# Performance work log

Hardware: AMD Instinct MI355X
Metric: run time of the kernel (lower is better)

## Reference

```python
import jax, jax.numpy as jnp
import numpy as np

HIDDEN = 1024
FFN = 2048
N_EXPERTS = 8
TOP_K = 2


def setup_inputs() -> dict:
    key = jax.random.key(0)
    k_x, k_g, k1, k2, k3 = jax.random.split(key, 5)
    hidden_states = jax.random.normal(k_x, (4, 4096, HIDDEN), dtype=jnp.float32)
    gate_w = jax.random.normal(k_g, (N_EXPERTS, HIDDEN), dtype=jnp.float32) * 0.02
    # nn.Linear convention: weight is [out_features, in_features]
    w1 = jax.random.normal(k1, (N_EXPERTS, FFN, HIDDEN), dtype=jnp.float32) * 0.02
    w2 = jax.random.normal(k2, (N_EXPERTS, HIDDEN, FFN), dtype=jnp.float32) * 0.02
    w3 = jax.random.normal(k3, (N_EXPERTS, FFN, HIDDEN), dtype=jnp.float32) * 0.02
    return {"hidden_states": hidden_states, "gate_w": gate_w, "w1": w1, "w2": w2, "w3": w3}


def reference(hidden_states, gate_w, w1, w2, w3):
    B, S, H = hidden_states.shape
    E = gate_w.shape[0]
    x = hidden_states.reshape(-1, H)  # [T, H]
    T = x.shape[0]

    # Router: softmax in fp32, top-2, renormalize (matches torch reference)
    router_logits = jnp.einsum("th,eh->te", x, gate_w)
    probs = jax.nn.softmax(router_logits.astype(jnp.float32), axis=-1)
    top_w, top_i = jax.lax.top_k(probs, TOP_K)  # [T, 2]
    top_w = top_w / jnp.sum(top_w, axis=-1, keepdims=True)
    top_w = top_w.astype(x.dtype)

    # Dense combine weights [T, E]: zero for unselected experts.
    combine = jnp.zeros((T, E), dtype=x.dtype)
    combine = combine.at[jnp.arange(T)[:, None], top_i].set(top_w)

    # Per-expert SwiGLU; loop over small fixed expert count, accumulate.
    out = jnp.zeros_like(x)
    for e in range(E):
        h = jax.nn.silu(x @ w1[e].T) * (x @ w3[e].T)  # [T, FFN]
        out = out + combine[:, e:e + 1] * (h @ w2[e].T)
    return out.reshape(B, S, H)
```

## Files before the change

kernel.cpp:

```cpp
#include <hip/hip_runtime.h>
#include <cstdint>

#define H 1024
#define F 2048
#define E_N 8
#define BM 256
#define BK 64
#define NW (E_N * F * H)

typedef __attribute__((ext_vector_type(8))) short short8v;
typedef __attribute__((ext_vector_type(4))) float float4v;
typedef unsigned short u16;

__device__ __forceinline__ u16 f2bf(float f) {
    uint32_t u = __float_as_uint(f);
    u += 0x7FFFu + ((u >> 16) & 1u);
    return (u16)(u >> 16);
}
__device__ __forceinline__ float bf2f(u16 b) {
    return __uint_as_float(((uint32_t)b) << 16);
}

__device__ __forceinline__ void gload16(const void* g, void* l) {
    __builtin_amdgcn_global_load_lds((const __attribute__((address_space(1))) uint32_t*)g,
                                     (__attribute__((address_space(3))) uint32_t*)l, 16, 0, 0);
}

__device__ __forceinline__ void barx() {
    asm volatile("" ::: "memory");
    __builtin_amdgcn_s_barrier();
    asm volatile("" ::: "memory");
}

__device__ __forceinline__ void decode_swz(int bid, int nTiles, int ngy, int gyc,
                                           int& tile, int& gy) {
    int nblk = nTiles * ngy;
    int q = nblk >> 3, r = nblk & 7;
    int xcd = bid & 7, pos = bid >> 3;
    int cid = (xcd < r ? xcd * (q + 1) : r * (q + 1) + (xcd - r) * q) + pos;
    int per = nTiles * gyc;
    int chunk = cid / per, rem = cid - chunk * per;
    tile = rem / gyc;
    gy = chunk * gyc + (rem - (rem / gyc) * gyc);
}

__global__ __launch_bounds__(256) void cvt3_kernel(const float* __restrict__ s0,
                                                   const float* __restrict__ s1,
                                                   const float* __restrict__ s2,
                                                   u16* __restrict__ dst) {
    int i = (blockIdx.x * 256 + threadIdx.x) * 4;
    int stride = gridDim.x * 256 * 4;
    for (; i < 3 * NW; i += stride) {
        int seg = i / NW;
        int off = i - seg * NW;
        const float* s = (seg == 0) ? s0 : ((seg == 1) ? s1 : s2);
        float4 v = *(const float4*)(s + off);
        ushort4 o;
        o.x = f2bf(v.x); o.y = f2bf(v.y); o.z = f2bf(v.z); o.w = f2bf(v.w);
        *(ushort4*)(dst + i) = o;
    }
}

__global__ __launch_bounds__(256) void router_kernel(const float* __restrict__ x,
                                                     const float* __restrict__ gw,
                                                     int* __restrict__ topi,
                                                     float* __restrict__ topw,
                                                     u16* __restrict__ xg, int T) {
    int wave = threadIdx.x >> 6, lane = threadIdx.x & 63;
    int t = blockIdx.x * 4 + wave;
    if (t >= T) return;
    const float4* xr = (const float4*)(x + (size_t)t * H);
    float4 xv[4];
#pragma unroll
    for (int i = 0; i < 4; i++) xv[i] = xr[i * 64 + lane];
#pragma unroll
    for (int i = 0; i < 4; i++) {
        ushort4 o;
        o.x = f2bf(xv[i].x); o.y = f2bf(xv[i].y);
        o.z = f2bf(xv[i].z); o.w = f2bf(xv[i].w);
        *(ushort4*)(xg + (size_t)t * H + (i * 64 + lane) * 4) = o;
    }
    float acc[E_N];
#pragma unroll
    for (int e = 0; e < E_N; e++) {
        const float4* gr = (const float4*)(gw + e * H);
        float s = 0.f;
#pragma unroll
        for (int i = 0; i < 4; i++) {
            float4 g = gr[i * 64 + lane];
            s += xv[i].x * g.x + xv[i].y * g.y + xv[i].z * g.z + xv[i].w * g.w;
        }
        acc[e] = s;
    }
#pragma unroll
    for (int e = 0; e < E_N; e++) {
#pragma unroll
        for (int off = 32; off; off >>= 1) acc[e] += __shfl_xor(acc[e], off, 64);
    }
    if (lane == 0) {
        int i0 = 0;
#pragma unroll
        for (int e = 1; e < E_N; e++) if (acc[e] > acc[i0]) i0 = e;
        int i1 = -1;
#pragma unroll
        for (int e = 0; e < E_N; e++) {
            if (e == i0) continue;
            if (i1 < 0 || acc[e] > acc[i1]) i1 = e;
        }
        float e1 = __expf(acc[i1] - acc[i0]);
        float w0 = 1.f / (1.f + e1);
        float w1v = e1 / (1.f + e1);
        topi[t * 2] = i0; topi[t * 2 + 1] = i1;
        topw[t * 2] = w0; topw[t * 2 + 1] = w1v;
    }
}

__global__ __launch_bounds__(256) void hist_kernel(const int* __restrict__ topi,
                                                   int* __restrict__ counts, int n) {
    __shared__ int hc[E_N];
    if (threadIdx.x < E_N) hc[threadIdx.x] = 0;
    __syncthreads();
    for (int i = blockIdx.x * 256 + threadIdx.x; i < n; i += gridDim.x * 256)
        atomicAdd(&hc[topi[i]], 1);
    __syncthreads();
    if (threadIdx.x < E_N) atomicAdd(&counts[threadIdx.x], hc[threadIdx.x]);
}

__global__ void scan_kernel(const int* __restrict__ counts, int* __restrict__ offsets,
                            int* __restrict__ cursors, int* __restrict__ tileOff) {
    if (threadIdx.x == 0 && blockIdx.x == 0) {
        int o = 0, to = 0;
        for (int e = 0; e < E_N; e++) {
            offsets[e] = o; cursors[e] = o; tileOff[e] = to;
            o += counts[e];
            to += (counts[e] + BM - 1) / BM;
        }
        offsets[E_N] = o; tileOff[E_N] = to;
    }
}

__global__ __launch_bounds__(1024) void scatter_kernel(const int* __restrict__ topi,
                                                       const float* __restrict__ topw,
                                                       int* __restrict__ cursors,
                                                       int* __restrict__ perm_tok,
                                                       float* __restrict__ perm_gate,
                                                       int* __restrict__ inv, int n) {
    __shared__ int hc[E_N];
    __shared__ int base[E_N];
    int tid = threadIdx.x;
    if (tid < E_N) hc[tid] = 0;
    __syncthreads();
    int i = blockIdx.x * 1024 + tid;
    int e = 0, lrank = 0;
    bool ok = (i < n);
    if (ok) {
        e = topi[i];
        lrank = atomicAdd(&hc[e], 1);
    }
    __syncthreads();
    if (tid < E_N) base[tid] = atomicAdd(&cursors[tid], hc[tid]);
    __syncthreads();
    if (ok) {
        int pos = base[e] + lrank;
        perm_tok[pos] = i >> 1;
        perm_gate[pos] = topw[i];
        inv[i] = pos;
    }
}

__global__ __launch_bounds__(512) void stage1_kernel(
    const u16* __restrict__ xg, const u16* __restrict__ w1b, const u16* __restrict__ w3b,
    const int* __restrict__ perm_tok, const float* __restrict__ perm_gate,
    const int* __restrict__ offsets, const int* __restrict__ tileOff,
    u16* __restrict__ h, int cstart, int tpcThis) {
    __shared__ u16 lA[2 * BM * BK];
    __shared__ u16 lB1[2 * 128 * BK];
    __shared__ u16 lB3[2 * 128 * BK];
    __shared__ int ptokS[BM];
    __shared__ float pgateS[BM];

    int tileL, nbIdx;
    decode_swz(blockIdx.x, tpcThis, F / 128, 4, tileL, nbIdx);
    int tile = cstart + tileL;
    if (tile >= tileOff[E_N]) return;
    int e = 0;
    while (e < E_N - 1 && tile >= tileOff[e + 1]) e++;
    int rbase = offsets[e] + (tile - tileOff[e]) * BM;
    int segEnd = offsets[e + 1];
    int e0 = 0;
    while (e0 < E_N - 1 && cstart >= tileOff[e0 + 1]) e0++;
    int chunkBase = offsets[e0] + (cstart - tileOff[e0]) * BM;

    int tid = threadIdx.x;
    if (tid < BM) {
        int p = rbase + tid; if (p > segEnd - 1) p = segEnd - 1;
        ptokS[tid] = perm_tok[p];
        pgateS[tid] = perm_gate[p];
    }
    __syncthreads();

    int lane = tid & 63, wid = tid >> 6;
    int wr = wid >> 2, wc = wid & 3;
    int lrow = lane & 15, kgrp = lane >> 4;
    int lr = lane >> 3, csw = ((lane & 7) ^ lr) << 3;
    int nb = nbIdx * 128;
    const u16* w1p = w1b + (size_t)e * F * H + (size_t)nb * H;
    const u16* w3p = w3b + (size_t)e * F * H + (size_t)nb * H;

    const u16* pA[4];
#pragma unroll
    for (int j = 0; j < 4; j++) pA[j] = xg + (size_t)ptokS[(j * 8 + wid) * 8 + lr] * H + csw;
    const u16 *pB1[2], *pB3[2];
#pragma unroll
    for (int j = 0; j < 2; j++) {
        int rr = (j * 8 + wid) * 8 + lr;
        pB1[j] = w1p + (size_t)rr * H + csw;
        pB3[j] = w3p + (size_t)rr * H + csw;
    }

    int swe0 = (kgrp ^ (lrow & 7)) << 3;
    int swe1 = ((4 + kgrp) ^ (lrow & 7)) << 3;
    int eA0 = (wr * 128 + lrow) * BK + swe0;
    int eA1 = (wr * 128 + lrow) * BK + swe1;
    int eB0 = (wc * 32 + lrow) * BK + swe0;
    int eB1 = (wc * 32 + lrow) * BK + swe1;

#define STA(CC, j)  gload16(pA[j],  &lA[(CC) * 16384 + ((j) * 8 + wid) * 8 * BK])
#define STB1(CC, j) gload16(pB1[j], &lB1[(CC) * 8192 + ((j) * 8 + wid) * 8 * BK])
#define STB3(CC, j) gload16(pB3[j], &lB3[(CC) * 8192 + ((j) * 8 + wid) * 8 * BK])

    float4v acc1[8][2], acc3[8][2];
#pragma unroll
    for (int a = 0; a < 8; a++)
#pragma unroll
        for (int b = 0; b < 2; b++) { acc1[a][b] = (float4v)(0.f); acc3[a][b] = (float4v)(0.f); }

    STB1(0, 0); STB1(0, 1);
    STB3(0, 0); STB3(0, 1);
    STA(0, 0); STA(0, 2); STA(0, 1); STA(0, 3);
#pragma unroll
    for (int j = 0; j < 4; j++) pA[j] += BK;
    pB1[0] += BK; pB1[1] += BK; pB3[0] += BK; pB3[1] += BK;
    asm volatile("s_waitcnt vmcnt(2)" ::: "memory");
    barx();

#define S1_DSA(CC, p) \
    short8v aF[2][2]; \
    _Pragma("unroll") \
    for (int pm = 0; pm < 2; pm++) { \
        aF[pm][0] = *(const short8v*)&lA[eA0 + (CC) * 16384 + (2 * (p) + pm) * 1024]; \
        aF[pm][1] = *(const short8v*)&lA[eA1 + (CC) * 16384 + (2 * (p) + pm) * 1024]; \
    }
#define S1_MM(p) \
    __builtin_amdgcn_s_setprio(1); \
    _Pragma("unroll") \
    for (int pm = 0; pm < 2; pm++) \
    _Pragma("unroll") \
    for (int n = 0; n < 2; n++) \
    _Pragma("unroll") \
    for (int kk = 0; kk < 2; kk++) { \
        acc1[2 * (p) + pm][n] = __builtin_amdgcn_mfma_f32_16x16x32_bf16(aF[pm][kk], b1F[n][kk], acc1[2 * (p) + pm][n], 0, 0, 0); \
        acc3[2 * (p) + pm][n] = __builtin_amdgcn_mfma_f32_16x16x32_bf16(aF[pm][kk], b3F[n][kk], acc3[2 * (p) + pm][n], 0, 0, 0); \
    } \
    __builtin_amdgcn_s_setprio(0);

#define S1_KT(CC, LAST) { \
    short8v b1F[2][2], b3F[2][2]; \
    _Pragma("unroll") \
    for (int n = 0; n < 2; n++) { \
        b1F[n][0] = *(const short8v*)&lB1[eB0 + (CC) * 8192 + n * 1024]; \
        b1F[n][1] = *(const short8v*)&lB1[eB1 + (CC) * 8192 + n * 1024]; \
        b3F[n][0] = *(const short8v*)&lB3[eB0 + (CC) * 8192 + n * 1024]; \
        b3F[n][1] = *(const short8v*)&lB3[eB1 + (CC) * 8192 + n * 1024]; \
    } \
    { S1_DSA(CC, 0) \
      if (!(LAST)) { STB1((CC) ^ 1, 0); STB1((CC) ^ 1, 1); STA((CC) ^ 1, 0); } \
      barx(); S1_MM(0) barx(); } \
    { S1_DSA(CC, 1) \
      if (!(LAST)) { STB3((CC) ^ 1, 0); STB3((CC) ^ 1, 1); STA((CC) ^ 1, 2); } \
      barx(); S1_MM(1) \
      if (!(LAST)) { asm volatile("s_waitcnt vmcnt(6)" ::: "memory"); } \
      else         { asm volatile("s_waitcnt vmcnt(0)" ::: "memory"); } \
      barx(); } \
    { S1_DSA(CC, 2) \
      if (!(LAST)) { STA((CC) ^ 1, 1); } \
      barx(); S1_MM(2) barx(); } \
    { S1_DSA(CC, 3) \
      if (!(LAST)) { STA((CC) ^ 1, 3); } \
      barx(); S1_MM(3) \
      asm volatile("s_waitcnt vmcnt(2)" ::: "memory"); \
      barx(); } \
    _Pragma("unroll") \
    for (int j = 0; j < 4; j++) pA[j] += BK; \
    pB1[0] += BK; pB1[1] += BK; pB3[0] += BK; pB3[1] += BK; \
}

    for (int tt = 0; tt < (H / BK) - 2; tt += 2) {
        S1_KT(0, false)
        S1_KT(1, false)
    }
    S1_KT(0, false)
    S1_KT(1, true)
#undef S1_DSA
#undef S1_MM
#undef S1_KT
#undef STA
#undef STB1
#undef STB3

    int rif = (lane >> 4) * 4;
#pragma unroll
    for (int m = 0; m < 8; m++) {
#pragma unroll
        for (int reg = 0; reg < 4; reg++) {
            int rowIdx = wr * 128 + m * 16 + rif + reg;
            int p = rbase + rowIdx;
            if (p < segEnd) {
                float g = pgateS[rowIdx];
#pragma unroll
                for (int n = 0; n < 2; n++) {
                    float a1 = acc1[m][n][reg], a3 = acc3[m][n][reg];
                    float sv = a1 / (1.f + __expf(-a1));
                    float hv = sv * a3 * g;
                    int ncol = nb + wc * 32 + n * 16 + (lane & 15);
                    h[(size_t)(p - chunkBase) * F + ncol] = f2bf(hv);
                }
            }
        }
    }
}

template<int NREP>
__global__ __launch_bounds__(512) void stage2_kernel(
    const u16* __restrict__ h, const u16* __restrict__ w2b,
    const int* __restrict__ offsets, const int* __restrict__ tileOff,
    u16* __restrict__ y, int cstart, int tpcThis) {
    constexpr int BN = NREP * 64;
    constexpr int BSTRIDE = BN * BK;
    __shared__ u16 lA[2 * BM * BK];
    __shared__ u16 lB[2 * BSTRIDE];

    int tileL, nbIdx;
    decode_swz(blockIdx.x, tpcThis, H / BN, 4, tileL, nbIdx);
    int tile = cstart + tileL;
    if (tile >= tileOff[E_N]) return;
    int e = 0;
    while (e < E_N - 1 && tile >= tileOff[e + 1]) e++;
    int rbase = offsets[e] + (tile - tileOff[e]) * BM;
    int segEnd = offsets[e + 1];
    int e0 = 0;
    while (e0 < E_N - 1 && cstart >= tileOff[e0 + 1]) e0++;
    int chunkBase = offsets[e0] + (cstart - tileOff[e0]) * BM;

    int tid = threadIdx.x;
    int lane = tid & 63, wid = tid >> 6;
    int wr = wid >> 2, wc = wid & 3;
    int lrow = lane & 15, kgrp = lane >> 4;
    int lr = lane >> 3, csw = ((lane & 7) ^ lr) << 3;
    int nb = nbIdx * BN;
    const u16* w2p = w2b + (size_t)e * H * F + (size_t)nb * F;

    const u16* pA[4];
#pragma unroll
    for (int j = 0; j < 4; j++) {
        int rb = (j * 8 + wid) * 8;
        int p = rbase + rb + lr; if (p > segEnd - 1) p = segEnd - 1;
        pA[j] = h + (size_t)(p - chunkBase) * F + csw;
    }
    const u16* pB[NREP];
#pragma unroll
    for (int j = 0; j < NREP; j++) pB[j] = w2p + (size_t)((j * 8 + wid) * 8 + lr) * F + csw;

    int swe0 = (kgrp ^ (lrow & 7)) << 3;
    int swe1 = ((4 + kgrp) ^ (lrow & 7)) << 3;
    int eA0 = (wr * 128 + lrow) * BK + swe0;
    int eA1 = (wr * 128 + lrow) * BK + swe1;
    int eB0 = (wc * (NREP * 16) + lrow) * BK + swe0;
    int eB1 = (wc * (NREP * 16) + lrow) * BK + swe1;

#define STA2(CC, j) gload16(pA[j], &lA[(CC) * 16384 + ((j) * 8 + wid) * 8 * BK])
#define STB2(CC, j) gload16(pB[j], &lB[(CC) * BSTRIDE + ((j) * 8 + wid) * 8 * BK])

    float4v acc[8][NREP];
#pragma unroll
    for (int a = 0; a < 8; a++)
#pragma unroll
        for (int b = 0; b < NREP; b++) acc[a][b] = (float4v)(0.f);

#pragma unroll
    for (int j = 0; j < NREP; j++) STB2(0, j);
    STA2(0, 0); STA2(0, 2); STA2(0, 1); STA2(0, 3);
#pragma unroll
    for (int j = 0; j < 4; j++) pA[j] += BK;
#pragma unroll
    for (int j = 0; j < NREP; j++) pB[j] += BK;
    asm volatile("s_waitcnt vmcnt(2)" ::: "memory");
    barx();

#define S2_DSA(CC, p) \
    short8v aF[2][2]; \
    _Pragma("unroll") \
    for (int pm = 0; pm < 2; pm++) { \
        aF[pm][0] = *(const short8v*)&lA[eA0 + (CC) * 16384 + (2 * (p) + pm) * 1024]; \
        aF[pm][1] = *(const short8v*)&lA[eA1 + (CC) * 16384 + (2 * (p) + pm) * 1024]; \
    }
#define S2_MM(p) \
    __builtin_amdgcn_s_setprio(1); \
    _Pragma("unroll") \
    for (int pm = 0; pm < 2; pm++) \
    _Pragma("unroll") \
    for (int n = 0; n < NREP; n++) \
    _Pragma("unroll") \
    for (int kk = 0; kk < 2; kk++) \
        acc[2 * (p) + pm][n] = __builtin_amdgcn_mfma_f32_16x16x32_bf16(aF[pm][kk], bF[n][kk], acc[2 * (p) + pm][n], 0, 0, 0); \
    __builtin_amdgcn_s_setprio(0);

#define S2_KT(CC, LAST) { \
    short8v bF[NREP][2]; \
    _Pragma("unroll") \
    for (int n = 0; n < NREP; n++) { \
        bF[n][0] = *(const short8v*)&lB[eB0 + (CC) * BSTRIDE + n * 1024]; \
        bF[n][1] = *(const short8v*)&lB[eB1 + (CC) * BSTRIDE + n * 1024]; \
    } \
    { S2_DSA(CC, 0) \
      if (!(LAST)) { STB2((CC) ^ 1, 0); if (NREP == 4) STB2((CC) ^ 1, 1); STA2((CC) ^ 1, 0); } \
      barx(); S2_MM(0) barx(); } \
    { S2_DSA(CC, 1) \
      if (!(LAST)) { if (NREP == 4) { STB2((CC) ^ 1, 2); STB2((CC) ^ 1, 3); } else STB2((CC) ^ 1, 1); \
                     STA2((CC) ^ 1, 2); } \
      barx(); S2_MM(1) \
      if (!(LAST)) { \
          if (NREP == 4) { asm volatile("s_waitcnt vmcnt(6)" ::: "memory"); } \
          else           { asm volatile("s_waitcnt vmcnt(4)" ::: "memory"); } \
      } else { asm volatile("s_waitcnt vmcnt(0)" ::: "memory"); } \
      barx(); } \
    { S2_DSA(CC, 2) \
      if (!(LAST)) { STA2((CC) ^ 1, 1); } \
      barx(); S2_MM(2) barx(); } \
    { S2_DSA(CC, 3) \
      if (!(LAST)) { STA2((CC) ^ 1, 3); } \
      barx(); S2_MM(3) \
      asm volatile("s_waitcnt vmcnt(2)" ::: "memory"); \
      barx(); } \
    _Pragma("unroll") \
    for (int j = 0; j < 4; j++) pA[j] += BK; \
    _Pragma("unroll") \
    for (int j = 0; j < NREP; j++) pB[j] += BK; \
}

    for (int tt = 0; tt < (F / BK) - 2; tt += 2) {
        S2_KT(0, false)
        S2_KT(1, false)
    }
    S2_KT(0, false)
    S2_KT(1, true)
#undef S2_DSA
#undef S2_MM
#undef S2_KT
#undef STA2
#undef STB2

    int rif = (lane >> 4) * 4;
#pragma unroll
    for (int m = 0; m < 8; m++) {
#pragma unroll
        for (int reg = 0; reg < 4; reg++) {
            int rowIdx = wr * 128 + m * 16 + rif + reg;
            int p = rbase + rowIdx;
            if (p < segEnd) {
#pragma unroll
                for (int n = 0; n < NREP; n++) {
                    int col = nb + wc * (BN / 4) + n * 16 + (lane & 15);
                    y[(size_t)p * H + col] = f2bf(acc[m][n][reg]);
                }
            }
        }
    }
}

__global__ __launch_bounds__(256) void combine_kernel(const u16* __restrict__ y,
                                                      const int* __restrict__ inv,
                                                      float* __restrict__ out) {
    int t = blockIdx.x, c = threadIdx.x;
    int s0 = inv[t * 2], s1 = inv[t * 2 + 1];
    ushort4 a = *(const ushort4*)(y + (size_t)s0 * H + c * 4);
    ushort4 b = *(const ushort4*)(y + (size_t)s1 * H + c * 4);
    float4 o;
    o.x = bf2f(a.x) + bf2f(b.x);
    o.y = bf2f(a.y) + bf2f(b.y);
    o.z = bf2f(a.z) + bf2f(b.z);
    o.w = bf2f(a.w) + bf2f(b.w);
    *(float4*)(out + (size_t)t * H + c * 4) = o;
}

extern "C" void kernel_launch(void* const* d_in, const int* in_sizes, int n_in,
                              void* d_out, int out_size, void* d_ws, size_t ws_size,
                              hipStream_t stream) {
    (void)n_in; (void)out_size;
    const float* x  = (const float*)d_in[0];
    const float* gw = (const float*)d_in[1];
    const float* w1 = (const float*)d_in[2];
    const float* w2 = (const float*)d_in[3];
    const float* w3 = (const float*)d_in[4];
    float* out = (float*)d_out;
    int T = in_sizes[0] / H;
    int P = T * 2;

    char* ws = (char*)d_ws;
    size_t off = 0;
    auto alloc = [&](size_t b) { size_t c = off; off = (off + b + 255) & ~(size_t)255; return c; };
    size_t misc_o  = alloc(256);
    int* counts  = (int*)(ws + misc_o);
    int* offsets = (int*)(ws + misc_o + 64);
    int* cursors = (int*)(ws + misc_o + 128);
    int* tileOff = (int*)(ws + misc_o + 192);
    size_t topi_o  = alloc((size_t)T * 2 * 4);
    size_t topw_o  = alloc((size_t)T * 2 * 4);
    size_t ptok_o  = alloc((size_t)P * 4);
    size_t pgate_o = alloc((size_t)P * 4);
    size_t inv_o   = alloc((size_t)T * 2 * 4);
    size_t wb_o  = alloc((size_t)3 * NW * 2);
    size_t xg_o  = alloc((size_t)T * H * 2);
    size_t y_o   = alloc((size_t)P * H * 2);
    u16* w1b = (u16*)(ws + wb_o);
    u16* w3b = w1b + NW;
    u16* w2b = w1b + 2 * (size_t)NW;

    int maxTiles = P / BM + E_N;
    size_t perTile = (size_t)BM * F * 2;
    size_t avail = (ws_size > off + 256) ? (ws_size - off - 256) : 0;
    int tpc = (int)(avail / perTile);
    if (tpc > maxTiles) tpc = maxTiles;
    if (tpc < 4) tpc = 4;
    size_t h_o = alloc((size_t)tpc * perTile);

    hipMemsetAsync(ws + misc_o, 0, 256, stream);

    cvt3_kernel<<<8192, 256, 0, stream>>>(w1, w3, w2, w1b);
    router_kernel<<<T / 4, 256, 0, stream>>>(x, gw, (int*)(ws + topi_o), (float*)(ws + topw_o),
                                             (u16*)(ws + xg_o), T);
    hist_kernel<<<32, 256, 0, stream>>>((int*)(ws + topi_o), counts, P);
    scan_kernel<<<1, 64, 0, stream>>>(counts, offsets, cursors, tileOff);
    scatter_kernel<<<(P + 1023) / 1024, 1024, 0, stream>>>(
        (int*)(ws + topi_o), (float*)(ws + topw_o), cursors,
        (int*)(ws + ptok_o), (float*)(ws + pgate_o), (int*)(ws + inv_o), P);

    for (int cstart = 0; cstart < maxTiles; cstart += tpc) {
        int tpcThis = maxTiles - cstart; if (tpcThis > tpc) tpcThis = tpc;
        stage1_kernel<<<tpcThis * (F / 128), 512, 0, stream>>>(
            (u16*)(ws + xg_o), w1b, w3b,
            (int*)(ws + ptok_o), (float*)(ws + pgate_o), offsets, tileOff,
            (u16*)(ws + h_o), cstart, tpcThis);
        if (tpcThis >= 54)
            stage2_kernel<4><<<tpcThis * (H / 256), 512, 0, stream>>>(
                (u16*)(ws + h_o), w2b, offsets, tileOff,
                (u16*)(ws + y_o), cstart, tpcThis);
        else
            stage2_kernel<2><<<tpcThis * (H / 128), 512, 0, stream>>>(
                (u16*)(ws + h_o), w2b, offsets, tileOff,
                (u16*)(ws + y_o), cstart, tpcThis);
    }
    combine_kernel<<<T, 256, 0, stream>>>((u16*)(ws + y_o), (int*)(ws + inv_o), out);
}
```

Measured before the change: 640.3 us.

## Switch stage1/stage2 GEMMs to 32x32x16 MFMA and balance chunk sizes

Replaces the 16x16x32 bf16 MFMA tiling in both expert GEMM kernels with 32x32x16 MFMA, restructuring LDS fragment loads, swizzle offsets, the K-loop into two half-phases with fewer barriers, and the epilogue row mapping. The larger MFMA needs fewer LDS fragment reads per FLOP and fewer instructions. The host also splits tiles evenly across chunks and changes the threshold for picking the wider stage2 variant. This risks higher register pressure from the 16-wide accumulators, and the epilogue writes are less coalesced.

After: 751.5 us. +17.4%, slower.

```diff
diff --git a/kernel.cpp b/kernel.cpp
--- a/kernel.cpp
+++ b/kernel.cpp
@@ -9,7 +9,7 @@
 #define NW (E_N * F * H)
 
 typedef __attribute__((ext_vector_type(8))) short short8v;
-typedef __attribute__((ext_vector_type(4))) float float4v;
+typedef __attribute__((ext_vector_type(16))) float float16v;
 typedef unsigned short u16;
 
 __device__ __forceinline__ u16 f2bf(float f) {
@@ -201,7 +201,7 @@
 
     int lane = tid & 63, wid = tid >> 6;
     int wr = wid >> 2, wc = wid & 3;
-    int lrow = lane & 15, kgrp = lane >> 4;
+    int l32 = lane & 31, hi = lane >> 5;
     int lr = lane >> 3, csw = ((lane & 7) ^ lr) << 3;
     int nb = nbIdx * 128;
     const u16* w1p = w1b + (size_t)e * F * H + (size_t)nb * H;
@@ -218,22 +218,19 @@
         pB3[j] = w3p + (size_t)rr * H + csw;
     }
 
-    int swe0 = (kgrp ^ (lrow & 7)) << 3;
-    int swe1 = ((4 + kgrp) ^ (lrow & 7)) << 3;
-    int eA0 = (wr * 128 + lrow) * BK + swe0;
-    int eA1 = (wr * 128 + lrow) * BK + swe1;
-    int eB0 = (wc * 32 + lrow) * BK + swe0;
-    int eB1 = (wc * 32 + lrow) * BK + swe1;
+    int uk[4];
+#pragma unroll
+    for (int k = 0; k < 4; k++) uk[k] = ((2 * k + hi) ^ (lane & 7)) << 3;
+    int aBase = (wr * 128 + l32) * BK;
+    int bBase = (wc * 32 + l32) * BK;
 
 #define STA(CC, j)  gload16(pA[j],  &lA[(CC) * 16384 + ((j) * 8 + wid) * 8 * BK])
 #define STB1(CC, j) gload16(pB1[j], &lB1[(CC) * 8192 + ((j) * 8 + wid) * 8 * BK])
 #define STB3(CC, j) gload16(pB3[j], &lB3[(CC) * 8192 + ((j) * 8 + wid) * 8 * BK])
 
-    float4v acc1[8][2], acc3[8][2];
-#pragma unroll
-    for (int a = 0; a < 8; a++)
-#pragma unroll
-        for (int b = 0; b < 2; b++) { acc1[a][b] = (float4v)(0.f); acc3[a][b] = (float4v)(0.f); }
+    float16v acc1[4], acc3[4];
+#pragma unroll
+    for (int a = 0; a < 4; a++) { acc1[a] = (float16v)(0.f); acc3[a] = (float16v)(0.f); }
 
     STB1(0, 0); STB1(0, 1);
     STB3(0, 0); STB3(0, 1);
@@ -244,52 +241,48 @@
     asm volatile("s_waitcnt vmcnt(2)" ::: "memory");
     barx();
 
-#define S1_DSA(CC, p) \
-    short8v aF[2][2]; \
-    _Pragma("unroll") \
-    for (int pm = 0; pm < 2; pm++) { \
-        aF[pm][0] = *(const short8v*)&lA[eA0 + (CC) * 16384 + (2 * (p) + pm) * 1024]; \
-        aF[pm][1] = *(const short8v*)&lA[eA1 + (CC) * 16384 + (2 * (p) + pm) * 1024]; \
-    }
-#define S1_MM(p) \
+#define S1_KT(CC, LAST) { \
+    short8v b1F[4], b3F[4], aF[2][4]; \
+    _Pragma("unroll") \
+    for (int k = 0; k < 4; k++) { \
+        b1F[k] = *(const short8v*)&lB1[(CC) * 8192 + bBase + uk[k]]; \
+        b3F[k] = *(const short8v*)&lB3[(CC) * 8192 + bBase + uk[k]]; \
+        aF[0][k] = *(const short8v*)&lA[(CC) * 16384 + aBase + uk[k]]; \
+        aF[1][k] = *(const short8v*)&lA[(CC) * 16384 + aBase + 2048 + uk[k]]; \
+    } \
+    if (!(LAST)) { STB1((CC) ^ 1, 0); STB1((CC) ^ 1, 1); STB3((CC) ^ 1, 0); STB3((CC) ^ 1, 1); \
+                   STA((CC) ^ 1, 0); STA((CC) ^ 1, 2); } \
+    barx(); \
     __builtin_amdgcn_s_setprio(1); \
     _Pragma("unroll") \
-    for (int pm = 0; pm < 2; pm++) \
-    _Pragma("unroll") \
-    for (int n = 0; n < 2; n++) \
-    _Pragma("unroll") \
-    for (int kk = 0; kk < 2; kk++) { \
-        acc1[2 * (p) + pm][n] = __builtin_amdgcn_mfma_f32_16x16x32_bf16(aF[pm][kk], b1F[n][kk], acc1[2 * (p) + pm][n], 0, 0, 0); \
-        acc3[2 * (p) + pm][n] = __builtin_amdgcn_mfma_f32_16x16x32_bf16(aF[pm][kk], b3F[n][kk], acc3[2 * (p) + pm][n], 0, 0, 0); \
-    } \
-    __builtin_amdgcn_s_setprio(0);
-
-#define S1_KT(CC, LAST) { \
-    short8v b1F[2][2], b3F[2][2]; \
-    _Pragma("unroll") \
-    for (int n = 0; n < 2; n++) { \
-        b1F[n][0] = *(const short8v*)&lB1[eB0 + (CC) * 8192 + n * 1024]; \
-        b1F[n][1] = *(const short8v*)&lB1[eB1 + (CC) * 8192 + n * 1024]; \
-        b3F[n][0] = *(const short8v*)&lB3[eB0 + (CC) * 8192 + n * 1024]; \
-        b3F[n][1] = *(const short8v*)&lB3[eB1 + (CC) * 8192 + n * 1024]; \
-    } \
-    { S1_DSA(CC, 0) \
-      if (!(LAST)) { STB1((CC) ^ 1, 0); STB1((CC) ^ 1, 1); STA((CC) ^ 1, 0); } \
-      barx(); S1_MM(0) barx(); } \
-    { S1_DSA(CC, 1) \
-      if (!(LAST)) { STB3((CC) ^ 1, 0); STB3((CC) ^ 1, 1); STA((CC) ^ 1, 2); } \
-      barx(); S1_MM(1) \
-      if (!(LAST)) { asm volatile("s_waitcnt vmcnt(6)" ::: "memory"); } \
-      else         { asm volatile("s_waitcnt vmcnt(0)" ::: "memory"); } \
-      barx(); } \
-    { S1_DSA(CC, 2) \
-      if (!(LAST)) { STA((CC) ^ 1, 1); } \
-      barx(); S1_MM(2) barx(); } \
-    { S1_DSA(CC, 3) \
-      if (!(LAST)) { STA((CC) ^ 1, 3); } \
-      barx(); S1_MM(3) \
-      asm volatile("s_waitcnt vmcnt(2)" ::: "memory"); \
-      barx(); } \
+    for (int k = 0; k < 4; k++) \
+    _Pragma("unroll") \
+    for (int mt = 0; mt < 2; mt++) { \
+        acc1[mt] = __builtin_amdgcn_mfma_f32_32x32x16_bf16(aF[mt][k], b1F[k], acc1[mt], 0, 0, 0); \
+        acc3[mt] = __builtin_amdgcn_mfma_f32_32x32x16_bf16(aF[mt][k], b3F[k], acc3[mt], 0, 0, 0); \
+    } \
+    __builtin_amdgcn_s_setprio(0); \
+    if (!(LAST)) { asm volatile("s_waitcnt vmcnt(6)" ::: "memory"); } \
+    else         { asm volatile("s_waitcnt vmcnt(0)" ::: "memory"); } \
+    barx(); \
+    _Pragma("unroll") \
+    for (int k = 0; k < 4; k++) { \
+        aF[0][k] = *(const short8v*)&lA[(CC) * 16384 + aBase + 2 * 2048 + uk[k]]; \
+        aF[1][k] = *(const short8v*)&lA[(CC) * 16384 + aBase + 3 * 2048 + uk[k]]; \
+    } \
+    if (!(LAST)) { STA((CC) ^ 1, 1); STA((CC) ^ 1, 3); } \
+    barx(); \
+    __builtin_amdgcn_s_setprio(1); \
+    _Pragma("unroll") \
+    for (int k = 0; k < 4; k++) \
+    _Pragma("unroll") \
+    for (int mt = 0; mt < 2; mt++) { \
+        acc1[2 + mt] = __builtin_amdgcn_mfma_f32_32x32x16_bf16(aF[mt][k], b1F[k], acc1[2 + mt], 0, 0, 0); \
+        acc3[2 + mt] = __builtin_amdgcn_mfma_f32_32x32x16_bf16(aF[mt][k], b3F[k], acc3[2 + mt], 0, 0, 0); \
+    } \
+    __builtin_amdgcn_s_setprio(0); \
+    asm volatile("s_waitcnt vmcnt(2)" ::: "memory"); \
+    barx(); \
     _Pragma("unroll") \
     for (int j = 0; j < 4; j++) pA[j] += BK; \
     pB1[0] += BK; pB1[1] += BK; pB3[0] += BK; pB3[1] += BK; \
@@ -301,30 +294,24 @@
     }
     S1_KT(0, false)
     S1_KT(1, true)
-#undef S1_DSA
-#undef S1_MM
 #undef S1_KT
 #undef STA
 #undef STB1
 #undef STB3
 
-    int rif = (lane >> 4) * 4;
-#pragma unroll
-    for (int m = 0; m < 8; m++) {
-#pragma unroll
-        for (int reg = 0; reg < 4; reg++) {
-            int rowIdx = wr * 128 + m * 16 + rif + reg;
+#pragma unroll
+    for (int mt = 0; mt < 4; mt++) {
+#pragma unroll
+        for (int r = 0; r < 16; r++) {
+            int rowIdx = wr * 128 + mt * 32 + (r & 3) + 8 * (r >> 2) + 4 * hi;
             int p = rbase + rowIdx;
             if (p < segEnd) {
                 float g = pgateS[rowIdx];
-#pragma unroll
-                for (int n = 0; n < 2; n++) {
-                    float a1 = acc1[m][n][reg], a3 = acc3[m][n][reg];
-                    float sv = a1 / (1.f + __expf(-a1));
-                    float hv = sv * a3 * g;
-                    int ncol = nb + wc * 32 + n * 16 + (lane & 15);
-                    h[(size_t)(p - chunkBase) * F + ncol] = f2bf(hv);
-                }
+                float a1 = acc1[mt][r], a3v = acc3[mt][r];
+                float sv = a1 / (1.f + __expf(-a1));
+                float hv = sv * a3v * g;
+                int ncol = nb + wc * 32 + l32;
+                h[(size_t)(p - chunkBase) * F + ncol] = f2bf(hv);
             }
         }
     }
@@ -337,6 +324,7 @@
     u16* __restrict__ y, int cstart, int tpcThis) {
     constexpr int BN = NREP * 64;
     constexpr int BSTRIDE = BN * BK;
+    constexpr int NT32 = NREP / 2;
     __shared__ u16 lA[2 * BM * BK];
     __shared__ u16 lB[2 * BSTRIDE];
 
@@ -355,7 +343,7 @@
     int tid = threadIdx.x;
     int lane = tid & 63, wid = tid >> 6;
     int wr = wid >> 2, wc = wid & 3;
-    int lrow = lane & 15, kgrp = lane >> 4;
+    int l32 = lane & 31, hi = lane >> 5;
     int lr = lane >> 3, csw = ((lane & 7) ^ lr) << 3;
     int nb = nbIdx * BN;
     const u16* w2p = w2b + (size_t)e * H * F + (size_t)nb * F;
@@ -371,21 +359,20 @@
 #pragma unroll
     for (int j = 0; j < NREP; j++) pB[j] = w2p + (size_t)((j * 8 + wid) * 8 + lr) * F + csw;
 
-    int swe0 = (kgrp ^ (lrow & 7)) << 3;
-    int swe1 = ((4 + kgrp) ^ (lrow & 7)) << 3;
-    int eA0 = (wr * 128 + lrow) * BK + swe0;
-    int eA1 = (wr * 128 + lrow) * BK + swe1;
-    int eB0 = (wc * (NREP * 16) + lrow) * BK + swe0;
-    int eB1 = (wc * (NREP * 16) + lrow) * BK + swe1;
+    int uk[4];
+#pragma unroll
+    for (int k = 0; k < 4; k++) uk[k] = ((2 * k + hi) ^ (lane & 7)) << 3;
+    int aBase = (wr * 128 + l32) * BK;
+    int bBase = (wc * (NREP * 16) + l32) * BK;
 
 #define STA2(CC, j) gload16(pA[j], &lA[(CC) * 16384 + ((j) * 8 + wid) * 8 * BK])
 #define STB2(CC, j) gload16(pB[j], &lB[(CC) * BSTRIDE + ((j) * 8 + wid) * 8 * BK])
 
-    float4v acc[8][NREP];
-#pragma unroll
-    for (int a = 0; a < 8; a++)
-#pragma unroll
-        for (int b = 0; b < NREP; b++) acc[a][b] = (float4v)(0.f);
+    float16v acc[4][NT32];
+#pragma unroll
+    for (int a = 0; a < 4; a++)
+#pragma unroll
+        for (int b = 0; b < NT32; b++) acc[a][b] = (float16v)(0.f);
 
 #pragma unroll
     for (int j = 0; j < NREP; j++) STB2(0, j);
@@ -397,51 +384,54 @@
     asm volatile("s_waitcnt vmcnt(2)" ::: "memory");
     barx();
 
-#define S2_DSA(CC, p) \
-    short8v aF[2][2]; \
-    _Pragma("unroll") \
-    for (int pm = 0; pm < 2; pm++) { \
-        aF[pm][0] = *(const short8v*)&lA[eA0 + (CC) * 16384 + (2 * (p) + pm) * 1024]; \
-        aF[pm][1] = *(const short8v*)&lA[eA1 + (CC) * 16384 + (2 * (p) + pm) * 1024]; \
-    }
-#define S2_MM(p) \
+#define S2_KT(CC, LAST) { \
+    short8v bF[NT32][4], aF[2][4]; \
+    _Pragma("unroll") \
+    for (int k = 0; k < 4; k++) { \
+        _Pragma("unroll") \
+        for (int nt = 0; nt < NT32; nt++) \
+            bF[nt][k] = *(const short8v*)&lB[(CC) * BSTRIDE + bBase + nt * 2048 + uk[k]]; \
+        aF[0][k] = *(const short8v*)&lA[(CC) * 16384 + aBase + uk[k]]; \
+        aF[1][k] = *(const short8v*)&lA[(CC) * 16384 + aBase + 2048 + uk[k]]; \
+    } \
+    if (!(LAST)) { \
+        _Pragma("unroll") \
+        for (int j = 0; j < NREP; j++) STB2((CC) ^ 1, j); \
+        STA2((CC) ^ 1, 0); STA2((CC) ^ 1, 2); \
+    } \
+    barx(); \
     __builtin_amdgcn_s_setprio(1); \
     _Pragma("unroll") \
-    for (int pm = 0; pm < 2; pm++) \
-    _Pragma("unroll") \
-    for (int n = 0; n < NREP; n++) \
-    _Pragma("unroll") \
-    for (int kk = 0; kk < 2; kk++) \
-        acc[2 * (p) + pm][n] = __builtin_amdgcn_mfma_f32_16x16x32_bf16(aF[pm][kk], bF[n][kk], acc[2 * (p) + pm][n], 0, 0, 0); \
-    __builtin_amdgcn_s_setprio(0);
-
-#define S2_KT(CC, LAST) { \
-    short8v bF[NREP][2]; \
-    _Pragma("unroll") \
-    for (int n = 0; n < NREP; n++) { \
-        bF[n][0] = *(const short8v*)&lB[eB0 + (CC) * BSTRIDE + n * 1024]; \
-        bF[n][1] = *(const short8v*)&lB[eB1 + (CC) * BSTRIDE + n * 1024]; \
-    } \
-    { S2_DSA(CC, 0) \
-      if (!(LAST)) { STB2((CC) ^ 1, 0); if (NREP == 4) STB2((CC) ^ 1, 1); STA2((CC) ^ 1, 0); } \
-      barx(); S2_MM(0) barx(); } \
-    { S2_DSA(CC, 1) \
-      if (!(LAST)) { if (NREP == 4) { STB2((CC) ^ 1, 2); STB2((CC) ^ 1, 3); } else STB2((CC) ^ 1, 1); \
-                     STA2((CC) ^ 1, 2); } \
-      barx(); S2_MM(1) \
-      if (!(LAST)) { \
-          if (NREP == 4) { asm volatile("s_waitcnt vmcnt(6)" ::: "memory"); } \
-          else           { asm volatile("s_waitcnt vmcnt(4)" ::: "memory"); } \
-      } else { asm volatile("s_waitcnt vmcnt(0)" ::: "memory"); } \
-      barx(); } \
-    { S2_DSA(CC, 2) \
-      if (!(LAST)) { STA2((CC) ^ 1, 1); } \
-      barx(); S2_MM(2) barx(); } \
-    { S2_DSA(CC, 3) \
-      if (!(LAST)) { STA2((CC) ^ 1, 3); } \
-      barx(); S2_MM(3) \
-      asm volatile("s_waitcnt vmcnt(2)" ::: "memory"); \
-      barx(); } \
+    for (int k = 0; k < 4; k++) \
+    _Pragma("unroll") \
+    for (int mt = 0; mt < 2; mt++) \
+    _Pragma("unroll") \
+    for (int nt = 0; nt < NT32; nt++) \
+        acc[mt][nt] = __builtin_amdgcn_mfma_f32_32x32x16_bf16(aF[mt][k], bF[nt][k], acc[mt][nt], 0, 0, 0); \
+    __builtin_amdgcn_s_setprio(0); \
+    if (!(LAST)) { \
+        if (NREP == 4) { asm volatile("s_waitcnt vmcnt(6)" ::: "memory"); } \
+        else           { asm volatile("s_waitcnt vmcnt(4)" ::: "memory"); } \
+    } else { asm volatile("s_waitcnt vmcnt(0)" ::: "memory"); } \
+    barx(); \
+    _Pragma("unroll") \
+    for (int k = 0; k < 4; k++) { \
+        aF[0][k] = *(const short8v*)&lA[(CC) * 16384 + aBase + 2 * 2048 + uk[k]]; \
+        aF[1][k] = *(const short8v*)&lA[(CC) * 16384 + aBase + 3 * 2048 + uk[k]]; \
+    } \
+    if (!(LAST)) { STA2((CC) ^ 1, 1); STA2((CC) ^ 1, 3); } \
+    barx(); \
+    __builtin_amdgcn_s_setprio(1); \
+    _Pragma("unroll") \
+    for (int k = 0; k < 4; k++) \
+    _Pragma("unroll") \
+    for (int mt = 0; mt < 2; mt++) \
+    _Pragma("unroll") \
+    for (int nt = 0; nt < NT32; nt++) \
+        acc[2 + mt][nt] = __builtin_amdgcn_mfma_f32_32x32x16_bf16(aF[mt][k], bF[nt][k], acc[2 + mt][nt], 0, 0, 0); \
+    __builtin_amdgcn_s_setprio(0); \
+    asm volatile("s_waitcnt vmcnt(2)" ::: "memory"); \
+    barx(); \
     _Pragma("unroll") \
     for (int j = 0; j < 4; j++) pA[j] += BK; \
     _Pragma("unroll") \
@@ -454,24 +444,21 @@
     }
     S2_KT(0, false)
     S2_KT(1, true)
-#undef S2_DSA
-#undef S2_MM
 #undef S2_KT
 #undef STA2
 #undef STB2
 
-    int rif = (lane >> 4) * 4;
-#pragma unroll
-    for (int m = 0; m < 8; m++) {
-#pragma unroll
-        for (int reg = 0; reg < 4; reg++) {
-            int rowIdx = wr * 128 + m * 16 + rif + reg;
-            int p = rbase + rowIdx;
-            if (p < segEnd) {
-#pragma unroll
-                for (int n = 0; n < NREP; n++) {
-                    int col = nb + wc * (BN / 4) + n * 16 + (lane & 15);
-                    y[(size_t)p * H + col] = f2bf(acc[m][n][reg]);
+#pragma unroll
+    for (int mt = 0; mt < 4; mt++) {
+#pragma unroll
+        for (int nt = 0; nt < NT32; nt++) {
+#pragma unroll
+            for (int r = 0; r < 16; r++) {
+                int rowIdx = wr * 128 + mt * 32 + (r & 3) + 8 * (r >> 2) + 4 * hi;
+                int p = rbase + rowIdx;
+                if (p < segEnd) {
+                    int col = nb + wc * (NREP * 16) + nt * 32 + l32;
+                    y[(size_t)p * H + col] = f2bf(acc[mt][nt][r]);
                 }
             }
         }
@@ -529,9 +516,11 @@
     int maxTiles = P / BM + E_N;
     size_t perTile = (size_t)BM * F * 2;
     size_t avail = (ws_size > off + 256) ? (ws_size - off - 256) : 0;
-    int tpc = (int)(avail / perTile);
-    if (tpc > maxTiles) tpc = maxTiles;
-    if (tpc < 4) tpc = 4;
+    int tpcMax = (int)(avail / perTile);
+    if (tpcMax > maxTiles) tpcMax = maxTiles;
+    if (tpcMax < 4) tpcMax = 4;
+    int nch = (maxTiles + tpcMax - 1) / tpcMax;
+    int tpc = (maxTiles + nch - 1) / nch;
     size_t h_o = alloc((size_t)tpc * perTile);
 
     hipMemsetAsync(ws + misc_o, 0, 256, stream);
@@ -551,7 +540,7 @@
             (u16*)(ws + xg_o), w1b, w3b,
             (int*)(ws + ptok_o), (float*)(ws + pgate_o), offsets, tileOff,
             (u16*)(ws + h_o), cstart, tpcThis);
-        if (tpcThis >= 54)
+        if (tpcThis * 4 >= 240)
             stage2_kernel<4><<<tpcThis * (H / 256), 512, 0, stream>>>(
                 (u16*)(ws + h_o), w2b, offsets, tileOff,
                 (u16*)(ws + y_o), cstart, tpcThis);
```

## Shrink stage1 tile to 128x64 with 256 threads and two blocks per CU

Applied to the files above, without the earlier changes.

The stage1 gate/up GEMM tile changes from 256x128 with 8 waves to 128x64 with 4 waves. Each 256-row routed tile is split into two halves and four times as many blocks are launched. The pipeline is simplified to two MFMA phases per K step, and launch bounds now request two blocks per CU to raise occupancy and improve load balance. The trade-off is less data reuse per block, so more global and LDS traffic per FLOP. The stage2 variant threshold is also rewritten (tpc*4>=240, equivalent to tpc>=60).

Result: no change. 643.9 us (+0.6%).

```diff
diff --git a/kernel.cpp b/kernel.cpp
--- a/kernel.cpp
+++ b/kernel.cpp
@@ -168,31 +168,32 @@
     }
 }
 
-__global__ __launch_bounds__(512) void stage1_kernel(
+__global__ __launch_bounds__(256, 2) void stage1_kernel(
     const u16* __restrict__ xg, const u16* __restrict__ w1b, const u16* __restrict__ w3b,
     const int* __restrict__ perm_tok, const float* __restrict__ perm_gate,
     const int* __restrict__ offsets, const int* __restrict__ tileOff,
     u16* __restrict__ h, int cstart, int tpcThis) {
-    __shared__ u16 lA[2 * BM * BK];
-    __shared__ u16 lB1[2 * 128 * BK];
-    __shared__ u16 lB3[2 * 128 * BK];
-    __shared__ int ptokS[BM];
-    __shared__ float pgateS[BM];
-
-    int tileL, nbIdx;
-    decode_swz(blockIdx.x, tpcThis, F / 128, 4, tileL, nbIdx);
+    __shared__ u16 lA[2 * 128 * BK];
+    __shared__ u16 lB1[2 * 64 * BK];
+    __shared__ u16 lB3[2 * 64 * BK];
+    __shared__ int ptokS[128];
+    __shared__ float pgateS[128];
+
+    int tileL, gy;
+    decode_swz(blockIdx.x, tpcThis, 64, 8, tileL, gy);
+    int half = gy >> 5, nbIdx = gy & 31;
     int tile = cstart + tileL;
     if (tile >= tileOff[E_N]) return;
     int e = 0;
     while (e < E_N - 1 && tile >= tileOff[e + 1]) e++;
-    int rbase = offsets[e] + (tile - tileOff[e]) * BM;
+    int rbase = offsets[e] + (tile - tileOff[e]) * BM + half * 128;
     int segEnd = offsets[e + 1];
     int e0 = 0;
     while (e0 < E_N - 1 && cstart >= tileOff[e0 + 1]) e0++;
     int chunkBase = offsets[e0] + (cstart - tileOff[e0]) * BM;
 
     int tid = threadIdx.x;
-    if (tid < BM) {
+    if (tid < 128) {
         int p = rbase + tid; if (p > segEnd - 1) p = segEnd - 1;
         ptokS[tid] = perm_tok[p];
         pgateS[tid] = perm_gate[p];
@@ -200,96 +201,100 @@
     __syncthreads();
 
     int lane = tid & 63, wid = tid >> 6;
-    int wr = wid >> 2, wc = wid & 3;
+    int wr = wid >> 1, wc = wid & 1;
     int lrow = lane & 15, kgrp = lane >> 4;
     int lr = lane >> 3, csw = ((lane & 7) ^ lr) << 3;
-    int nb = nbIdx * 128;
+    int nb = nbIdx * 64;
     const u16* w1p = w1b + (size_t)e * F * H + (size_t)nb * H;
     const u16* w3p = w3b + (size_t)e * F * H + (size_t)nb * H;
 
+    int gA[4];
+#pragma unroll
+    for (int j = 0; j < 4; j++) gA[j] = (j & 1) * 8 + (j >> 1) * 4 + wid;
+
     const u16* pA[4];
 #pragma unroll
-    for (int j = 0; j < 4; j++) pA[j] = xg + (size_t)ptokS[(j * 8 + wid) * 8 + lr] * H + csw;
+    for (int j = 0; j < 4; j++) pA[j] = xg + (size_t)ptokS[gA[j] * 8 + lr] * H + csw;
     const u16 *pB1[2], *pB3[2];
 #pragma unroll
     for (int j = 0; j < 2; j++) {
-        int rr = (j * 8 + wid) * 8 + lr;
+        int rr = (j * 4 + wid) * 8 + lr;
         pB1[j] = w1p + (size_t)rr * H + csw;
         pB3[j] = w3p + (size_t)rr * H + csw;
     }
 
     int swe0 = (kgrp ^ (lrow & 7)) << 3;
     int swe1 = ((4 + kgrp) ^ (lrow & 7)) << 3;
-    int eA0 = (wr * 128 + lrow) * BK + swe0;
-    int eA1 = (wr * 128 + lrow) * BK + swe1;
+    int eA0 = (wr * 64 + lrow) * BK + swe0;
+    int eA1 = (wr * 64 + lrow) * BK + swe1;
     int eB0 = (wc * 32 + lrow) * BK + swe0;
     int eB1 = (wc * 32 + lrow) * BK + swe1;
 
-#define STA(CC, j)  gload16(pA[j],  &lA[(CC) * 16384 + ((j) * 8 + wid) * 8 * BK])
-#define STB1(CC, j) gload16(pB1[j], &lB1[(CC) * 8192 + ((j) * 8 + wid) * 8 * BK])
-#define STB3(CC, j) gload16(pB3[j], &lB3[(CC) * 8192 + ((j) * 8 + wid) * 8 * BK])
-
-    float4v acc1[8][2], acc3[8][2];
-#pragma unroll
-    for (int a = 0; a < 8; a++)
+#define STA(CC, j)  gload16(pA[j],  &lA[(CC) * 8192 + gA[j] * 8 * BK])
+#define STB1(CC, j) gload16(pB1[j], &lB1[(CC) * 4096 + ((j) * 4 + wid) * 8 * BK])
+#define STB3(CC, j) gload16(pB3[j], &lB3[(CC) * 4096 + ((j) * 4 + wid) * 8 * BK])
+
+    float4v acc1[4][2], acc3[4][2];
+#pragma unroll
+    for (int a = 0; a < 4; a++)
 #pragma unroll
         for (int b = 0; b < 2; b++) { acc1[a][b] = (float4v)(0.f); acc3[a][b] = (float4v)(0.f); }
 
-    STB1(0, 0); STB1(0, 1);
-    STB3(0, 0); STB3(0, 1);
-    STA(0, 0); STA(0, 2); STA(0, 1); STA(0, 3);
+    STB1(0, 0); STB1(0, 1); STB3(0, 0); STB3(0, 1);
+    STA(0, 0); STA(0, 1);
+    STA(0, 2); STA(0, 3);
 #pragma unroll
     for (int j = 0; j < 4; j++) pA[j] += BK;
     pB1[0] += BK; pB1[1] += BK; pB3[0] += BK; pB3[1] += BK;
     asm volatile("s_waitcnt vmcnt(2)" ::: "memory");
     barx();
 
-#define S1_DSA(CC, p) \
-    short8v aF[2][2]; \
-    _Pragma("unroll") \
-    for (int pm = 0; pm < 2; pm++) { \
-        aF[pm][0] = *(const short8v*)&lA[eA0 + (CC) * 16384 + (2 * (p) + pm) * 1024]; \
-        aF[pm][1] = *(const short8v*)&lA[eA1 + (CC) * 16384 + (2 * (p) + pm) * 1024]; \
-    }
-#define S1_MM(p) \
+#define S1_MM(MB, AFR) \
     __builtin_amdgcn_s_setprio(1); \
     _Pragma("unroll") \
-    for (int pm = 0; pm < 2; pm++) \
+    for (int m = 0; m < 2; m++) \
     _Pragma("unroll") \
     for (int n = 0; n < 2; n++) \
     _Pragma("unroll") \
     for (int kk = 0; kk < 2; kk++) { \
-        acc1[2 * (p) + pm][n] = __builtin_amdgcn_mfma_f32_16x16x32_bf16(aF[pm][kk], b1F[n][kk], acc1[2 * (p) + pm][n], 0, 0, 0); \
-        acc3[2 * (p) + pm][n] = __builtin_amdgcn_mfma_f32_16x16x32_bf16(aF[pm][kk], b3F[n][kk], acc3[2 * (p) + pm][n], 0, 0, 0); \
+        acc1[(MB) + m][n] = __builtin_amdgcn_mfma_f32_16x16x32_bf16(AFR[m][kk], b1F[n][kk], acc1[(MB) + m][n], 0, 0, 0); \
+        acc3[(MB) + m][n] = __builtin_amdgcn_mfma_f32_16x16x32_bf16(AFR[m][kk], b3F[n][kk], acc3[(MB) + m][n], 0, 0, 0); \
     } \
     __builtin_amdgcn_s_setprio(0);
 
 #define S1_KT(CC, LAST) { \
-    short8v b1F[2][2], b3F[2][2]; \
+    short8v b1F[2][2], b3F[2][2], aF[2][2]; \
     _Pragma("unroll") \
     for (int n = 0; n < 2; n++) { \
-        b1F[n][0] = *(const short8v*)&lB1[eB0 + (CC) * 8192 + n * 1024]; \
-        b1F[n][1] = *(const short8v*)&lB1[eB1 + (CC) * 8192 + n * 1024]; \
-        b3F[n][0] = *(const short8v*)&lB3[eB0 + (CC) * 8192 + n * 1024]; \
-        b3F[n][1] = *(const short8v*)&lB3[eB1 + (CC) * 8192 + n * 1024]; \
+        b1F[n][0] = *(const short8v*)&lB1[(CC) * 4096 + eB0 + n * 1024]; \
+        b1F[n][1] = *(const short8v*)&lB1[(CC) * 4096 + eB1 + n * 1024]; \
+        b3F[n][0] = *(const short8v*)&lB3[(CC) * 4096 + eB0 + n * 1024]; \
+        b3F[n][1] = *(const short8v*)&lB3[(CC) * 4096 + eB1 + n * 1024]; \
     } \
-    { S1_DSA(CC, 0) \
-      if (!(LAST)) { STB1((CC) ^ 1, 0); STB1((CC) ^ 1, 1); STA((CC) ^ 1, 0); } \
-      barx(); S1_MM(0) barx(); } \
-    { S1_DSA(CC, 1) \
-      if (!(LAST)) { STB3((CC) ^ 1, 0); STB3((CC) ^ 1, 1); STA((CC) ^ 1, 2); } \
-      barx(); S1_MM(1) \
-      if (!(LAST)) { asm volatile("s_waitcnt vmcnt(6)" ::: "memory"); } \
-      else         { asm volatile("s_waitcnt vmcnt(0)" ::: "memory"); } \
-      barx(); } \
-    { S1_DSA(CC, 2) \
-      if (!(LAST)) { STA((CC) ^ 1, 1); } \
-      barx(); S1_MM(2) barx(); } \
-    { S1_DSA(CC, 3) \
-      if (!(LAST)) { STA((CC) ^ 1, 3); } \
-      barx(); S1_MM(3) \
-      asm volatile("s_waitcnt vmcnt(2)" ::: "memory"); \
-      barx(); } \
+    _Pragma("unroll") \
+    for (int m = 0; m < 2; m++) { \
+        aF[m][0] = *(const short8v*)&lA[(CC) * 8192 + eA0 + m * 1024]; \
+        aF[m][1] = *(const short8v*)&lA[(CC) * 8192 + eA1 + m * 1024]; \
+    } \
+    if (!(LAST)) { STB1((CC) ^ 1, 0); STB1((CC) ^ 1, 1); STB3((CC) ^ 1, 0); STB3((CC) ^ 1, 1); \
+                   STA((CC) ^ 1, 0); STA((CC) ^ 1, 1); } \
+    barx(); \
+    S1_MM(0, aF) \
+    if (!(LAST)) { asm volatile("s_waitcnt vmcnt(6)" ::: "memory"); } \
+    else         { asm volatile("s_waitcnt vmcnt(0)" ::: "memory"); } \
+    barx(); \
+    short8v aG[2][2]; \
+    _Pragma("unroll") \
+    for (int m = 0; m < 2; m++) { \
+        aG[m][0] = *(const short8v*)&lA[(CC) * 8192 + eA0 + (2 + m) * 1024]; \
+        aG[m][1] = *(const short8v*)&lA[(CC) * 8192 + eA1 + (2 + m) * 1024]; \
+    } \
+    if (!(LAST)) { STA((CC) ^ 1, 2); STA((CC) ^ 1, 3); } \
+    barx(); \
+    S1_MM(2, aG) \
+    if (!(LAST)) { asm volatile("s_waitcnt vmcnt(2)" ::: "memory"); } \
+    else         { asm volatile("s_waitcnt vmcnt(0)" ::: "memory"); } \
+    barx(); \
     _Pragma("unroll") \
     for (int j = 0; j < 4; j++) pA[j] += BK; \
     pB1[0] += BK; pB1[1] += BK; pB3[0] += BK; pB3[1] += BK; \
@@ -301,19 +306,18 @@
     }
     S1_KT(0, false)
     S1_KT(1, true)
-#undef S1_DSA
+#undef S1_KT
 #undef S1_MM
-#undef S1_KT
 #undef STA
 #undef STB1
 #undef STB3
 
     int rif = (lane >> 4) * 4;
 #pragma unroll
-    for (int m = 0; m < 8; m++) {
+    for (int m = 0; m < 4; m++) {
 #pragma unroll
         for (int reg = 0; reg < 4; reg++) {
-            int rowIdx = wr * 128 + m * 16 + rif + reg;
+            int rowIdx = wr * 64 + m * 16 + rif + reg;
             int p = rbase + rowIdx;
             if (p < segEnd) {
                 float g = pgateS[rowIdx];
@@ -547,11 +551,11 @@
 
     for (int cstart = 0; cstart < maxTiles; cstart += tpc) {
         int tpcThis = maxTiles - cstart; if (tpcThis > tpc) tpcThis = tpc;
-        stage1_kernel<<<tpcThis * (F / 128), 512, 0, stream>>>(
+        stage1_kernel<<<tpcThis * 64, 256, 0, stream>>>(
             (u16*)(ws + xg_o), w1b, w3b,
             (int*)(ws + ptok_o), (float*)(ws + pgate_o), offsets, tileOff,
             (u16*)(ws + h_o), cstart, tpcThis);
-        if (tpcThis >= 54)
+        if (tpcThis * 4 >= 240)
             stage2_kernel<4><<<tpcThis * (H / 256), 512, 0, stream>>>(
                 (u16*)(ws + h_o), w2b, offsets, tileOff,
                 (u16*)(ws + y_o), cstart, tpcThis);
```
